# Kernel optimization log

Hardware: AMD Instinct MI355X
Metric: run time of the kernel (lower is better)

The kernel has to match this reference:

```python
import jax, jax.numpy as jnp
import numpy as np

N, H, O, E, K = 131072, 128, 128, 8, 2


def setup_inputs() -> dict:
    key = jax.random.key(0)
    k1, k2, k3, k4 = jax.random.split(key, 4)
    x = jax.random.normal(k1, (N, H), dtype=jnp.float32)
    w_gate = jax.random.normal(k2, (H, E), dtype=jnp.float32) * 0.02
    w_noise = jax.random.normal(k3, (H, E), dtype=jnp.float32) * 0.02
    w_expert = jax.random.normal(k4, (E, H, O), dtype=jnp.float32) * (1.0 / np.sqrt(H))
    b_expert = jnp.zeros((E, O), dtype=jnp.float32)
    return {"x": x, "w_gate": w_gate, "w_noise": w_noise,
            "w_expert": w_expert, "b_expert": b_expert, "top_k": K}


def _gates(x, w_gate, top_k):
    # Noisy top-k gating (eval mode: noise term w_noise is inactive).
    logits = x @ w_gate                              # [N, E]
    top_vals, top_idx = jax.lax.top_k(logits, top_k)  # [N, K]
    top_gates = jax.nn.softmax(top_vals, axis=-1)     # renormalize over top-k
    n = logits.shape[0]
    rows = jnp.arange(n)[:, None]                     # [N, 1]
    gates = jnp.zeros_like(logits).at[rows, top_idx].set(top_gates)  # [N, E] sparse
    return gates


def reference(x, w_gate, w_noise, w_expert, b_expert, top_k):
    gates = _gates(x, w_gate, top_k)                                  # [N, E]
    # Dense (mathematically identical) dispatch/combine: every expert FFN
    # applied per token, weighted by its (mostly-zero) gate.
    expert_out = jnp.einsum('nh,eho->neo', x, w_expert) + b_expert     # [N, E, O]
    out = jnp.einsum('ne,neo->no', gates, expert_out)                  # [N, O]
    return out
```

## Files before the change

kernel.cpp:

```cpp
#include <hip/hip_runtime.h>
#include <math.h>

typedef __bf16 bf16x8 __attribute__((ext_vector_type(8)));
typedef float f32x16 __attribute__((ext_vector_type(16)));

#define NTOK 131072
#define HDIM 128
#define ODIM 128
#define NEXP 8

__device__ __forceinline__ unsigned short f2bf(float f){
  union { float f; unsigned u; } v; v.f = f;
  unsigned r = v.u + 0x7FFFu + ((v.u >> 16) & 1u);
  return (unsigned short)(r >> 16);
}

__global__ void pack_w(const float* __restrict__ we, unsigned short* __restrict__ pw){
  int f = blockIdx.x * 256 + threadIdx.x;
  int l   = f & 63;
  int kt2 = (f >> 6) & 3;
  int e   = (f >> 8) & 7;
  int h   = (f >> 11) & 1;
  int ot  = (f >> 12) & 3;
  int o = ot * 32 + (l & 31);
  int kbase = (h * 4 + kt2) * 16 + ((l >> 5) << 3);
  unsigned short vals[8];
#pragma unroll
  for (int j = 0; j < 8; ++j)
    vals[j] = f2bf(we[(e * HDIM + kbase + j) * ODIM + o]);
  *(bf16x8*)(pw + (size_t)f * 8) = *(bf16x8*)vals;
}

__global__ void gating_pack(const float* __restrict__ x, const float* __restrict__ wg,
                            float* __restrict__ gates_t, unsigned short* __restrict__ xf){
  __shared__ float xs[64 * 128];
  __shared__ float wgl[128 * 8];
  __shared__ float plg[64 * 36];
  int t = threadIdx.x;
  size_t tokbase = (size_t)blockIdx.x * 64;

  ((float4*)wgl)[t] = ((const float4*)wg)[t];
  {
    const float4* xsrc = (const float4*)(x + tokbase * HDIM);
#pragma unroll
    for (int i = 0; i < 8; ++i){
      int idx = i * 256 + t;
      int tok = idx >> 5, c = idx & 31;
      *(float4*)&xs[tok * 128 + ((c ^ (tok & 7)) << 2)] = xsrc[idx];
    }
  }
  __syncthreads();

  {
    int tok = t & 63, q = t >> 6;
    float lg[8];
#pragma unroll
    for (int e = 0; e < 8; ++e) lg[e] = 0.0f;
#pragma unroll
    for (int i = 0; i < 8; ++i){
      int c = q * 8 + i;
      float4 v = *(float4*)&xs[tok * 128 + ((c ^ (tok & 7)) << 2)];
      const float* wr = wgl + c * 32;
#pragma unroll
      for (int e = 0; e < 8; ++e)
        lg[e] += v.x * wr[e] + v.y * wr[8 + e] + v.z * wr[16 + e] + v.w * wr[24 + e];
    }
    *(float4*)&plg[tok * 36 + q * 8]     = make_float4(lg[0], lg[1], lg[2], lg[3]);
    *(float4*)&plg[tok * 36 + q * 8 + 4] = make_float4(lg[4], lg[5], lg[6], lg[7]);
  }
  __syncthreads();

  if (t < 64){
    float lg[8];
#pragma unroll
    for (int e = 0; e < 8; ++e)
      lg[e] = plg[t * 36 + e] + plg[t * 36 + 8 + e] + plg[t * 36 + 16 + e] + plg[t * 36 + 24 + e];
    int i1 = 0; float v1 = lg[0];
#pragma unroll
    for (int e = 1; e < 8; ++e) if (lg[e] > v1){ v1 = lg[e]; i1 = e; }
    int i2 = -1; float v2 = -3.4e38f;
#pragma unroll
    for (int e = 0; e < 8; ++e) if (e != i1 && lg[e] > v2){ v2 = lg[e]; i2 = e; }
    float ex = __expf(v2 - v1);
    float inv = 1.0f / (1.0f + ex);
#pragma unroll
    for (int e = 0; e < 8; ++e)
      gates_t[(size_t)e * NTOK + tokbase + t] = (e == i1) ? inv : ((e == i2) ? ex * inv : 0.0f);
  }

  {
    int tokL = t >> 2, q = t & 3;
    float4 cv[8];
#pragma unroll
    for (int i = 0; i < 8; ++i)
      cv[i] = *(float4*)&xs[tokL * 128 + (((q * 8 + i) ^ (tokL & 7)) << 2)];
    size_t tgG = (size_t)blockIdx.x * 2 + (tokL >> 5);
#pragma unroll
    for (int jb = 0; jb < 4; ++jb){
      int h0 = q * 32 + jb * 8;
      int kt = h0 >> 4;
      int lslot = (tokL & 31) + 32 * (jb & 1);
      float4 a = cv[2 * jb], b = cv[2 * jb + 1];
      unsigned long long lo = (unsigned long long)f2bf(a.x)
                            | ((unsigned long long)f2bf(a.y) << 16)
                            | ((unsigned long long)f2bf(a.z) << 32)
                            | ((unsigned long long)f2bf(a.w) << 48);
      unsigned long long hi = (unsigned long long)f2bf(b.x)
                            | ((unsigned long long)f2bf(b.y) << 16)
                            | ((unsigned long long)f2bf(b.z) << 32)
                            | ((unsigned long long)f2bf(b.w) << 48);
      unsigned long long* dst = (unsigned long long*)(xf + ((tgG * 8 + kt) * 64 + lslot) * 8);
      dst[0] = lo; dst[1] = hi;
    }
  }
}

__launch_bounds__(256, 4)
__global__ void moe_gemm(const unsigned short* __restrict__ pw,
                         const unsigned short* __restrict__ xf,
                         const float* __restrict__ gates_t,
                         const float* __restrict__ be, float* __restrict__ out){
  __shared__ unsigned short Wh[16384];
  __shared__ float blds[256];

  int t = threadIdx.x;
  int ot = blockIdx.x & 3;
  int tb = blockIdx.x >> 2;
  int w = t >> 6, l = t & 63, l32 = l & 31, lh = l >> 5;
  size_t tokb = (size_t)tb * 256;

  blds[t] = be[(t >> 5) * ODIM + ot * 32 + (t & 31)];

  f32x16 zero16;
#pragma unroll
  for (int i = 0; i < 16; ++i) zero16[i] = 0.0f;
  f32x16 tot0 = zero16, tot1 = zero16;

#pragma unroll 1
  for (int h = 0; h < 2; ++h){
    {
      const uint4* wsrc = (const uint4*)(pw + (size_t)(ot * 2 + h) * 16384);
      uint4* wdst = (uint4*)Wh;
#pragma unroll
      for (int it = 0; it < 8; ++it)
        wdst[it * 256 + t] = wsrc[it * 256 + t];
    }
    bf16x8 xb0[4], xb1[4];
    {
      size_t tgG = tokb / 32 + w * 2;
#pragma unroll
      for (int kt = 0; kt < 4; ++kt){
        xb0[kt] = *(const bf16x8*)(xf + (((tgG + 0) * 8 + h * 4 + kt) * 64 + l) * 8);
        xb1[kt] = *(const bf16x8*)(xf + (((tgG + 1) * 8 + h * 4 + kt) * 64 + l) * 8);
      }
    }
    __syncthreads();

#pragma unroll 1
    for (int e = 0; e < 8; ++e){
      float g0 = gates_t[(size_t)e * NTOK + tokb + (w * 2 + 0) * 32 + l32];
      float g1 = gates_t[(size_t)e * NTOK + tokb + (w * 2 + 1) * 32 + l32];
      f32x16 p0 = zero16, p1 = zero16;
#pragma unroll
      for (int kt = 0; kt < 4; ++kt){
        bf16x8 a = *(const bf16x8*)&Wh[((e * 4 + kt) * 64 + l) * 8];
        p0 = __builtin_amdgcn_mfma_f32_32x32x16_bf16(a, xb0[kt], p0, 0, 0, 0);
        p1 = __builtin_amdgcn_mfma_f32_32x32x16_bf16(a, xb1[kt], p1, 0, 0, 0);
      }
#pragma unroll
      for (int r = 0; r < 16; ++r){ tot0[r] += g0 * p0[r]; tot1[r] += g1 * p1[r]; }
    }
    __syncthreads();
  }

#pragma unroll
  for (int e = 0; e < 8; ++e){
    float g0 = gates_t[(size_t)e * NTOK + tokb + (w * 2 + 0) * 32 + l32];
    float g1 = gates_t[(size_t)e * NTOK + tokb + (w * 2 + 1) * 32 + l32];
#pragma unroll
    for (int rg = 0; rg < 4; ++rg){
      float4 b4 = *(float4*)&blds[e * 32 + rg * 8 + lh * 4];
      tot0[rg * 4 + 0] += g0 * b4.x; tot0[rg * 4 + 1] += g0 * b4.y;
      tot0[rg * 4 + 2] += g0 * b4.z; tot0[rg * 4 + 3] += g0 * b4.w;
      tot1[rg * 4 + 0] += g1 * b4.x; tot1[rg * 4 + 1] += g1 * b4.y;
      tot1[rg * 4 + 2] += g1 * b4.z; tot1[rg * 4 + 3] += g1 * b4.w;
    }
  }
  {
    float* orow0 = out + (tokb + (size_t)(w * 2 + 0) * 32 + l32) * ODIM + ot * 32;
    float* orow1 = out + (tokb + (size_t)(w * 2 + 1) * 32 + l32) * ODIM + ot * 32;
#pragma unroll
    for (int rg = 0; rg < 4; ++rg){
      *(float4*)(orow0 + rg * 8 + lh * 4) =
        make_float4(tot0[rg * 4 + 0], tot0[rg * 4 + 1], tot0[rg * 4 + 2], tot0[rg * 4 + 3]);
      *(float4*)(orow1 + rg * 8 + lh * 4) =
        make_float4(tot1[rg * 4 + 0], tot1[rg * 4 + 1], tot1[rg * 4 + 2], tot1[rg * 4 + 3]);
    }
  }
}

extern "C" void kernel_launch(void* const* d_in, const int* in_sizes, int n_in,
                              void* d_out, int out_size, void* d_ws, size_t ws_size,
                              hipStream_t stream){
  const float* x  = (const float*)d_in[0];
  const float* wg = (const float*)d_in[1];
  const float* we = (const float*)d_in[3];
  const float* be = (const float*)d_in[4];
  float* out = (float*)d_out;

  unsigned short* pw      = (unsigned short*)d_ws;
  float*          gates_t = (float*)((char*)d_ws + 262144);
  unsigned short* xf      = (unsigned short*)((char*)d_ws + 4456448);

  pack_w     <<<64,   256, 0, stream>>>(we, pw);
  gating_pack<<<2048, 256, 0, stream>>>(x, wg, gates_t, xf);
  moe_gemm   <<<2048, 256, 0, stream>>>(pw, xf, gates_t, be, out);
}
```

Before: 165.8 us.

## Make MoE GEMM persistent with full-K resident weights and double-buffered token loads

The repacked expert weights now hold the full K dimension (8 k-tiles) in one 64KB LDS tile per output slice, loaded once per block. Each block then loops over 32 token groups (1024 tokens) instead of 256, with register double-buffering of x fragments and gates so the next group's loads overlap the current MFMA work. This removes the repeated weight reload, the half-K split with its barriers, and the per-expert gate reloads. In exchange the grid drops to 512 blocks, occupancy is capped at 2 blocks per CU, and register pressure rises from two 8-entry fragment buffers.

```diff
diff --git a/kernel.cpp b/kernel.cpp
--- a/kernel.cpp
+++ b/kernel.cpp
@@ -17,13 +17,12 @@
 
 __global__ void pack_w(const float* __restrict__ we, unsigned short* __restrict__ pw){
   int f = blockIdx.x * 256 + threadIdx.x;
-  int l   = f & 63;
-  int kt2 = (f >> 6) & 3;
-  int e   = (f >> 8) & 7;
-  int h   = (f >> 11) & 1;
-  int ot  = (f >> 12) & 3;
+  int l  = f & 63;
+  int kt = (f >> 6) & 7;
+  int e  = (f >> 9) & 7;
+  int ot = (f >> 12) & 3;
   int o = ot * 32 + (l & 31);
-  int kbase = (h * 4 + kt2) * 16 + ((l >> 5) << 3);
+  int kbase = kt * 16 + ((l >> 5) << 3);
   unsigned short vals[8];
 #pragma unroll
   for (int j = 0; j < 8; ++j)
@@ -115,88 +114,94 @@
   }
 }
 
-__launch_bounds__(256, 4)
+__launch_bounds__(256, 2)
 __global__ void moe_gemm(const unsigned short* __restrict__ pw,
                          const unsigned short* __restrict__ xf,
                          const float* __restrict__ gates_t,
                          const float* __restrict__ be, float* __restrict__ out){
-  __shared__ unsigned short Wh[16384];
+  __shared__ unsigned short Wh[8 * 8 * 64 * 8];
   __shared__ float blds[256];
 
   int t = threadIdx.x;
   int ot = blockIdx.x & 3;
   int tb = blockIdx.x >> 2;
   int w = t >> 6, l = t & 63, l32 = l & 31, lh = l >> 5;
-  size_t tokb = (size_t)tb * 256;
-
+  size_t tgG0 = (size_t)tb * 32;
+
+  {
+    const uint4* wsrc = (const uint4*)pw + (size_t)ot * 4096;
+    uint4* wdst = (uint4*)Wh;
+#pragma unroll
+    for (int i = 0; i < 16; ++i)
+      wdst[i * 256 + t] = wsrc[i * 256 + t];
+  }
   blds[t] = be[(t >> 5) * ODIM + ot * 32 + (t & 31)];
+  __syncthreads();
 
   f32x16 zero16;
 #pragma unroll
   for (int i = 0; i < 16; ++i) zero16[i] = 0.0f;
-  f32x16 tot0 = zero16, tot1 = zero16;
-
+
+#define LOADF(XB, G, TG)                                                        \
+  {                                                                             \
+    size_t tgG_ = tgG0 + (TG);                                                  \
+    _Pragma("unroll")                                                           \
+    for (int kt = 0; kt < 8; ++kt)                                              \
+      XB[kt] = *(const bf16x8*)(xf + ((tgG_ * 8 + kt) * 64 + l) * 8);           \
+    _Pragma("unroll")                                                           \
+    for (int e = 0; e < 8; ++e)                                                 \
+      G[e] = gates_t[(size_t)e * NTOK + tgG_ * 32 + l32];                       \
+  }
+
+#define COMPUTE_STORE(XB, G, TG)                                                \
+  {                                                                             \
+    f32x16 tot = zero16;                                                        \
+    _Pragma("unroll")                                                           \
+    for (int e = 0; e < 8; e += 2){                                             \
+      f32x16 p0 = zero16, p1 = zero16;                                          \
+      _Pragma("unroll")                                                         \
+      for (int kt = 0; kt < 8; ++kt){                                           \
+        bf16x8 a0 = *(const bf16x8*)&Wh[(((e + 0) * 8 + kt) * 64 + l) * 8];     \
+        bf16x8 a1 = *(const bf16x8*)&Wh[(((e + 1) * 8 + kt) * 64 + l) * 8];     \
+        p0 = __builtin_amdgcn_mfma_f32_32x32x16_bf16(a0, XB[kt], p0, 0, 0, 0);  \
+        p1 = __builtin_amdgcn_mfma_f32_32x32x16_bf16(a1, XB[kt], p1, 0, 0, 0);  \
+      }                                                                         \
+      _Pragma("unroll")                                                         \
+      for (int r = 0; r < 16; ++r)                                              \
+        tot[r] += G[e] * p0[r] + G[e + 1] * p1[r];                              \
+    }                                                                           \
+    _Pragma("unroll")                                                           \
+    for (int e = 0; e < 8; ++e){                                                \
+      _Pragma("unroll")                                                         \
+      for (int rg = 0; rg < 4; ++rg){                                           \
+        float4 b4 = *(float4*)&blds[e * 32 + rg * 8 + lh * 4];                  \
+        tot[rg * 4 + 0] += G[e] * b4.x; tot[rg * 4 + 1] += G[e] * b4.y;         \
+        tot[rg * 4 + 2] += G[e] * b4.z; tot[rg * 4 + 3] += G[e] * b4.w;         \
+      }                                                                         \
+    }                                                                           \
+    float* orow = out + ((tgG0 + (TG)) * 32 + l32) * ODIM + ot * 32;            \
+    _Pragma("unroll")                                                           \
+    for (int rg = 0; rg < 4; ++rg)                                              \
+      *(float4*)(orow + rg * 8 + lh * 4) =                                      \
+        make_float4(tot[rg * 4 + 0], tot[rg * 4 + 1],                           \
+                    tot[rg * 4 + 2], tot[rg * 4 + 3]);                          \
+  }
+
+  bf16x8 xbA[8], xbB[8];
+  float gA[8], gB[8];
+  LOADF(xbA, gA, w)
 #pragma unroll 1
-  for (int h = 0; h < 2; ++h){
-    {
-      const uint4* wsrc = (const uint4*)(pw + (size_t)(ot * 2 + h) * 16384);
-      uint4* wdst = (uint4*)Wh;
-#pragma unroll
-      for (int it = 0; it < 8; ++it)
-        wdst[it * 256 + t] = wsrc[it * 256 + t];
-    }
-    bf16x8 xb0[4], xb1[4];
-    {
-      size_t tgG = tokb / 32 + w * 2;
-#pragma unroll
-      for (int kt = 0; kt < 4; ++kt){
-        xb0[kt] = *(const bf16x8*)(xf + (((tgG + 0) * 8 + h * 4 + kt) * 64 + l) * 8);
-        xb1[kt] = *(const bf16x8*)(xf + (((tgG + 1) * 8 + h * 4 + kt) * 64 + l) * 8);
-      }
-    }
-    __syncthreads();
-
-#pragma unroll 1
-    for (int e = 0; e < 8; ++e){
-      float g0 = gates_t[(size_t)e * NTOK + tokb + (w * 2 + 0) * 32 + l32];
-      float g1 = gates_t[(size_t)e * NTOK + tokb + (w * 2 + 1) * 32 + l32];
-      f32x16 p0 = zero16, p1 = zero16;
-#pragma unroll
-      for (int kt = 0; kt < 4; ++kt){
-        bf16x8 a = *(const bf16x8*)&Wh[((e * 4 + kt) * 64 + l) * 8];
-        p0 = __builtin_amdgcn_mfma_f32_32x32x16_bf16(a, xb0[kt], p0, 0, 0, 0);
-        p1 = __builtin_amdgcn_mfma_f32_32x32x16_bf16(a, xb1[kt], p1, 0, 0, 0);
-      }
-#pragma unroll
-      for (int r = 0; r < 16; ++r){ tot0[r] += g0 * p0[r]; tot1[r] += g1 * p1[r]; }
-    }
-    __syncthreads();
-  }
-
-#pragma unroll
-  for (int e = 0; e < 8; ++e){
-    float g0 = gates_t[(size_t)e * NTOK + tokb + (w * 2 + 0) * 32 + l32];
-    float g1 = gates_t[(size_t)e * NTOK + tokb + (w * 2 + 1) * 32 + l32];
-#pragma unroll
-    for (int rg = 0; rg < 4; ++rg){
-      float4 b4 = *(float4*)&blds[e * 32 + rg * 8 + lh * 4];
-      tot0[rg * 4 + 0] += g0 * b4.x; tot0[rg * 4 + 1] += g0 * b4.y;
-      tot0[rg * 4 + 2] += g0 * b4.z; tot0[rg * 4 + 3] += g0 * b4.w;
-      tot1[rg * 4 + 0] += g1 * b4.x; tot1[rg * 4 + 1] += g1 * b4.y;
-      tot1[rg * 4 + 2] += g1 * b4.z; tot1[rg * 4 + 3] += g1 * b4.w;
-    }
-  }
-  {
-    float* orow0 = out + (tokb + (size_t)(w * 2 + 0) * 32 + l32) * ODIM + ot * 32;
-    float* orow1 = out + (tokb + (size_t)(w * 2 + 1) * 32 + l32) * ODIM + ot * 32;
-#pragma unroll
-    for (int rg = 0; rg < 4; ++rg){
-      *(float4*)(orow0 + rg * 8 + lh * 4) =
-        make_float4(tot0[rg * 4 + 0], tot0[rg * 4 + 1], tot0[rg * 4 + 2], tot0[rg * 4 + 3]);
-      *(float4*)(orow1 + rg * 8 + lh * 4) =
-        make_float4(tot1[rg * 4 + 0], tot1[rg * 4 + 1], tot1[rg * 4 + 2], tot1[rg * 4 + 3]);
-    }
-  }
+  for (int it2 = 0; it2 < 4; ++it2){
+    int tgA = it2 * 8 + w;
+    int tgB = it2 * 8 + 4 + w;
+    LOADF(xbB, gB, tgB)
+    COMPUTE_STORE(xbA, gA, tgA)
+    int tgA2 = (it2 < 3) ? (it2 * 8 + 8 + w) : tgA;
+    LOADF(xbA, gA, tgA2)
+    COMPUTE_STORE(xbB, gB, tgB)
+  }
+#undef LOADF
+#undef COMPUTE_STORE
 }
 
 extern "C" void kernel_launch(void* const* d_in, const int* in_sizes, int n_in,
@@ -214,5 +219,5 @@
 
   pack_w     <<<64,   256, 0, stream>>>(we, pw);
   gating_pack<<<2048, 256, 0, stream>>>(x, wg, gates_t, xf);
-  moe_gemm   <<<2048, 256, 0, stream>>>(pw, xf, gates_t, be, out);
-}
+  moe_gemm   <<<512,  256, 0, stream>>>(pw, xf, gates_t, be, out);
+}
```

Result: slower. 603.4 us (+263.9%).

## Load full expert weight slice once per block and loop over token tiles

Applied to the files above, without the earlier changes.

The GEMM kernel now loads the whole 128-deep weight slice for all experts (64KB LDS) once per block, then loops over 8 token groups per wave. The old version reloaded half-slices twice per 256-token block with syncs. The grid shrinks to 512 blocks, and each token tile is processed with the full K dimension and two experts interleaved per MFMA chain. This amortizes the weight loads and removes the barriers, at the cost of lower occupancy (launch bounds 2, larger LDS) and fewer blocks per CU.

```diff
diff --git a/kernel.cpp b/kernel.cpp
--- a/kernel.cpp
+++ b/kernel.cpp
@@ -17,13 +17,12 @@
 
 __global__ void pack_w(const float* __restrict__ we, unsigned short* __restrict__ pw){
   int f = blockIdx.x * 256 + threadIdx.x;
-  int l   = f & 63;
-  int kt2 = (f >> 6) & 3;
-  int e   = (f >> 8) & 7;
-  int h   = (f >> 11) & 1;
-  int ot  = (f >> 12) & 3;
+  int l  = f & 63;
+  int kt = (f >> 6) & 7;
+  int e  = (f >> 9) & 7;
+  int ot = (f >> 12) & 3;
   int o = ot * 32 + (l & 31);
-  int kbase = (h * 4 + kt2) * 16 + ((l >> 5) << 3);
+  int kbase = kt * 16 + ((l >> 5) << 3);
   unsigned short vals[8];
 #pragma unroll
   for (int j = 0; j < 8; ++j)
@@ -115,87 +114,78 @@
   }
 }
 
-__launch_bounds__(256, 4)
+__launch_bounds__(256, 2)
 __global__ void moe_gemm(const unsigned short* __restrict__ pw,
                          const unsigned short* __restrict__ xf,
                          const float* __restrict__ gates_t,
                          const float* __restrict__ be, float* __restrict__ out){
-  __shared__ unsigned short Wh[16384];
+  __shared__ unsigned short Wh[8 * 8 * 64 * 8];
   __shared__ float blds[256];
 
   int t = threadIdx.x;
   int ot = blockIdx.x & 3;
   int tb = blockIdx.x >> 2;
   int w = t >> 6, l = t & 63, l32 = l & 31, lh = l >> 5;
-  size_t tokb = (size_t)tb * 256;
-
+  size_t tgG0 = (size_t)tb * 32;
+
+  {
+    const uint4* wsrc = (const uint4*)pw + (size_t)ot * 4096;
+    uint4* wdst = (uint4*)Wh;
+#pragma unroll
+    for (int i = 0; i < 16; ++i)
+      wdst[i * 256 + t] = wsrc[i * 256 + t];
+  }
   blds[t] = be[(t >> 5) * ODIM + ot * 32 + (t & 31)];
+  __syncthreads();
 
   f32x16 zero16;
 #pragma unroll
   for (int i = 0; i < 16; ++i) zero16[i] = 0.0f;
-  f32x16 tot0 = zero16, tot1 = zero16;
 
 #pragma unroll 1
-  for (int h = 0; h < 2; ++h){
-    {
-      const uint4* wsrc = (const uint4*)(pw + (size_t)(ot * 2 + h) * 16384);
-      uint4* wdst = (uint4*)Wh;
-#pragma unroll
-      for (int it = 0; it < 8; ++it)
-        wdst[it * 256 + t] = wsrc[it * 256 + t];
-    }
-    bf16x8 xb0[4], xb1[4];
-    {
-      size_t tgG = tokb / 32 + w * 2;
-#pragma unroll
-      for (int kt = 0; kt < 4; ++kt){
-        xb0[kt] = *(const bf16x8*)(xf + (((tgG + 0) * 8 + h * 4 + kt) * 64 + l) * 8);
-        xb1[kt] = *(const bf16x8*)(xf + (((tgG + 1) * 8 + h * 4 + kt) * 64 + l) * 8);
+  for (int it = 0; it < 8; ++it){
+    size_t tgG = tgG0 + it * 4 + w;
+
+    bf16x8 xb[8];
+#pragma unroll
+    for (int kt = 0; kt < 8; ++kt)
+      xb[kt] = *(const bf16x8*)(xf + ((tgG * 8 + kt) * 64 + l) * 8);
+    float g[8];
+#pragma unroll
+    for (int e = 0; e < 8; ++e)
+      g[e] = gates_t[(size_t)e * NTOK + tgG * 32 + l32];
+
+    f32x16 tot = zero16;
+#pragma unroll
+    for (int e = 0; e < 8; e += 2){
+      f32x16 p0 = zero16, p1 = zero16;
+#pragma unroll
+      for (int kt = 0; kt < 8; ++kt){
+        bf16x8 a0 = *(const bf16x8*)&Wh[(((e + 0) * 8 + kt) * 64 + l) * 8];
+        bf16x8 a1 = *(const bf16x8*)&Wh[(((e + 1) * 8 + kt) * 64 + l) * 8];
+        p0 = __builtin_amdgcn_mfma_f32_32x32x16_bf16(a0, xb[kt], p0, 0, 0, 0);
+        p1 = __builtin_amdgcn_mfma_f32_32x32x16_bf16(a1, xb[kt], p1, 0, 0, 0);
       }
-    }
-    __syncthreads();
-
-#pragma unroll 1
+#pragma unroll
+      for (int r = 0; r < 16; ++r)
+        tot[r] += g[e] * p0[r] + g[e + 1] * p1[r];
+    }
+
+#pragma unroll
     for (int e = 0; e < 8; ++e){
-      float g0 = gates_t[(size_t)e * NTOK + tokb + (w * 2 + 0) * 32 + l32];
-      float g1 = gates_t[(size_t)e * NTOK + tokb + (w * 2 + 1) * 32 + l32];
-      f32x16 p0 = zero16, p1 = zero16;
-#pragma unroll
-      for (int kt = 0; kt < 4; ++kt){
-        bf16x8 a = *(const bf16x8*)&Wh[((e * 4 + kt) * 64 + l) * 8];
-        p0 = __builtin_amdgcn_mfma_f32_32x32x16_bf16(a, xb0[kt], p0, 0, 0, 0);
-        p1 = __builtin_amdgcn_mfma_f32_32x32x16_bf16(a, xb1[kt], p1, 0, 0, 0);
+#pragma unroll
+      for (int rg = 0; rg < 4; ++rg){
+        float4 b4 = *(float4*)&blds[e * 32 + rg * 8 + lh * 4];
+        tot[rg * 4 + 0] += g[e] * b4.x; tot[rg * 4 + 1] += g[e] * b4.y;
+        tot[rg * 4 + 2] += g[e] * b4.z; tot[rg * 4 + 3] += g[e] * b4.w;
       }
-#pragma unroll
-      for (int r = 0; r < 16; ++r){ tot0[r] += g0 * p0[r]; tot1[r] += g1 * p1[r]; }
-    }
-    __syncthreads();
-  }
-
-#pragma unroll
-  for (int e = 0; e < 8; ++e){
-    float g0 = gates_t[(size_t)e * NTOK + tokb + (w * 2 + 0) * 32 + l32];
-    float g1 = gates_t[(size_t)e * NTOK + tokb + (w * 2 + 1) * 32 + l32];
-#pragma unroll
-    for (int rg = 0; rg < 4; ++rg){
-      float4 b4 = *(float4*)&blds[e * 32 + rg * 8 + lh * 4];
-      tot0[rg * 4 + 0] += g0 * b4.x; tot0[rg * 4 + 1] += g0 * b4.y;
-      tot0[rg * 4 + 2] += g0 * b4.z; tot0[rg * 4 + 3] += g0 * b4.w;
-      tot1[rg * 4 + 0] += g1 * b4.x; tot1[rg * 4 + 1] += g1 * b4.y;
-      tot1[rg * 4 + 2] += g1 * b4.z; tot1[rg * 4 + 3] += g1 * b4.w;
-    }
-  }
-  {
-    float* orow0 = out + (tokb + (size_t)(w * 2 + 0) * 32 + l32) * ODIM + ot * 32;
-    float* orow1 = out + (tokb + (size_t)(w * 2 + 1) * 32 + l32) * ODIM + ot * 32;
-#pragma unroll
-    for (int rg = 0; rg < 4; ++rg){
-      *(float4*)(orow0 + rg * 8 + lh * 4) =
-        make_float4(tot0[rg * 4 + 0], tot0[rg * 4 + 1], tot0[rg * 4 + 2], tot0[rg * 4 + 3]);
-      *(float4*)(orow1 + rg * 8 + lh * 4) =
-        make_float4(tot1[rg * 4 + 0], tot1[rg * 4 + 1], tot1[rg * 4 + 2], tot1[rg * 4 + 3]);
-    }
+    }
+
+    float* orow = out + (tgG * 32 + l32) * ODIM + ot * 32;
+#pragma unroll
+    for (int rg = 0; rg < 4; ++rg)
+      *(float4*)(orow + rg * 8 + lh * 4) =
+        make_float4(tot[rg * 4 + 0], tot[rg * 4 + 1], tot[rg * 4 + 2], tot[rg * 4 + 3]);
   }
 }
 
@@ -214,5 +204,5 @@
 
   pack_w     <<<64,   256, 0, stream>>>(we, pw);
   gating_pack<<<2048, 256, 0, stream>>>(x, wg, gates_t, xf);
-  moe_gemm   <<<2048, 256, 0, stream>>>(pw, xf, gates_t, be, out);
-}
+  moe_gemm   <<<512,  256, 0, stream>>>(pw, xf, gates_t, be, out);
+}
```

Result: slower. 394.1 us (+137.7%).
